# Kernel tuning notes

Hardware: AMD Instinct MI355X
Metric: run time of the kernel (lower is better)

The kernel has to match this reference:

```python
import jax, jax.numpy as jnp
import numpy as np

RATE = 2
KSIZE = 3
STRIDE = 1
SOFTMAX_SCALE = 10.0
EPS_NAN = 1e-4


def resize_bilinear_align(x, oh, ow):
    # torch F.interpolate(mode='bilinear', align_corners=True)
    B, C, H, W = x.shape
    ys = jnp.linspace(0.0, H - 1.0, oh)
    xs = jnp.linspace(0.0, W - 1.0, ow)
    y0 = jnp.floor(ys).astype(jnp.int32)
    y1 = jnp.minimum(y0 + 1, H - 1)
    wy = (ys - y0).astype(x.dtype)
    x0 = jnp.floor(xs).astype(jnp.int32)
    x1 = jnp.minimum(x0 + 1, W - 1)
    wx = (xs - x0).astype(x.dtype)
    t = x[:, :, y0, :] * (1 - wy)[None, None, :, None] + x[:, :, y1, :] * wy[None, None, :, None]
    return t[:, :, :, x0] * (1 - wx) + t[:, :, :, x1] * wx


def extract_patches(x, k, s, pad):
    # x: [C,H,W] -> [L, C, k, k] with SAME padding (pad on each side), L = oh*ow
    C, H, W = x.shape
    xp = jnp.pad(x, ((0, 0), (pad, pad), (pad, pad)))
    oh = (H + 2 * pad - k) // s + 1
    ow = (W + 2 * pad - k) // s + 1
    cols = jnp.stack(
        [xp[:, i:i + s * (oh - 1) + 1:s, j:j + s * (ow - 1) + 1:s]
         for i in range(k) for j in range(k)], axis=0)  # [k*k, C, oh, ow]
    return cols.reshape(k, k, C, oh, ow).transpose(3, 4, 2, 0, 1).reshape(oh * ow, C, k, k)


def conv2d(x, w, padding):
    # x: [N,C,H,W], w: [O,I,kh,kw]
    return jax.lax.conv_general_dilated(
        x, w, (1, 1), [(padding, padding)] * 2,
        dimension_numbers=('NCHW', 'OIHW', 'NCHW'))


def conv_transpose2d(x, w, stride, padding):
    # torch conv_transpose2d: x [N,I,h,w], w [I,O,kh,kw]
    k = w.shape[2]
    wt = jnp.flip(w, (2, 3)).transpose(1, 0, 2, 3)  # [O,I,kh,kw]
    return jax.lax.conv_general_dilated(
        x, wt, (1, 1), [(k - 1 - padding, k - 1 - padding)] * 2,
        lhs_dilation=(stride, stride),
        dimension_numbers=('NCHW', 'OIHW', 'NCHW'))


def setup_inputs() -> dict:
    key = jax.random.key(0)
    k1, k2 = jax.random.split(key)
    B, C, H, W = 4, 64, 128, 128
    background = jax.random.normal(k1, (B, C, H, W), dtype=jnp.float32)
    foreground = jax.random.normal(k2, (B, C, H, W), dtype=jnp.float32)
    return {"background": background, "foreground": foreground}


def reference(background, foreground):
    B, C, H, W = background.shape
    h, w = H // RATE, W // RATE
    fg = resize_bilinear_align(foreground, h, w)  # [B,C,h,w]
    bks = 2 * RATE  # background patch kernel = 4

    def per_sample(fg_i, bg_i):
        # foreground patches [L,C,3,3], L = h*w
        fgp = extract_patches(fg_i, KSIZE, STRIDE, 1)
        norm = jnp.sqrt(jnp.sum(fgp * fgp, axis=(1, 2, 3), keepdims=True))
        fgp_n = fgp / jnp.maximum(norm, EPS_NAN)
        # correlation score [1,L,h,w]
        score = conv2d(fg_i[None], fgp_n, padding=1)
        attn = jax.nn.softmax(score * SOFTMAX_SCALE, axis=1)
        attn = jnp.clip(attn, 1e-8, None)
        # background patches [L,C,4,4] (kernel 4, stride 2, same-pad 1)
        bgp = extract_patches(bg_i, bks, STRIDE * RATE, 1)
        out = conv_transpose2d(attn, bgp, stride=RATE, padding=1) / 4.0
        return out[0]  # [C,H,W]

    return jax.vmap(per_sample)(fg, background)
```

## Files before the change

kernel.cpp:

```cpp
#include <hip/hip_runtime.h>
#include <hip/hip_bf16.h>
#include <math.h>

#define B_  4
#define C_  64
#define H_  128
#define W_  128
#define HS  64
#define WS  64
#define L_  4096
#define K1  576
#define E2  1024
#define KSPLIT 1
#define ZLOG (-17.5f)

typedef _Float16 f16;
typedef f16 f16x8 __attribute__((ext_vector_type(8)));
typedef float f32x4 __attribute__((ext_vector_type(4)));

__device__ __forceinline__ void gload16(const void* g, void* l) {
    __builtin_amdgcn_global_load_lds(
        (const __attribute__((address_space(1))) unsigned int*)g,
        (__attribute__((address_space(3))) unsigned int*)l, 16, 0, 0);
}

__device__ __forceinline__ int swz(int r, int c) {
    return r * 128 + ((((c >> 3) ^ (r & 7)) << 3) | (c & 7));
}

__global__ __launch_bounds__(256) void resize_kernel(const float* __restrict__ fg,
                                                     float* __restrict__ fgs) {
    int idx = blockIdx.x * 256 + threadIdx.x;
    if (idx >= B_ * C_ * HS * WS) return;
    int j = idx & 63, i = (idx >> 6) & 63, bc = idx >> 12;
    const float sc = 127.0f / 63.0f;
    float yf = i * sc, xf = j * sc;
    int y0 = (int)floorf(yf); if (y0 > 127) y0 = 127;
    int x0 = (int)floorf(xf); if (x0 > 127) x0 = 127;
    int y1 = min(y0 + 1, 127), x1 = min(x0 + 1, 127);
    float wy = yf - (float)y0, wx = xf - (float)x0;
    const float* p = fg + (size_t)bc * (H_ * W_);
    float a = p[y0 * W_ + x0], b = p[y0 * W_ + x1];
    float c = p[y1 * W_ + x0], d = p[y1 * W_ + x1];
    float t0 = a * (1.f - wy) + c * wy;
    float t1 = b * (1.f - wy) + d * wy;
    fgs[idx] = t0 * (1.f - wx) + t1 * wx;
}

__global__ __launch_bounds__(256) void patch_kernel(const float* __restrict__ fgs,
                                                    f16* __restrict__ P_all) {
    int idx = blockIdx.x * 256 + threadIdx.x;
    int b = blockIdx.y;
    int k = idx % K1, l = idx / K1;
    int c = k / 9, r = k % 9;
    int dy = r / 3, dx = r % 3;
    int ly = l >> 6, lx = l & 63;
    int y = ly - 1 + dy, x = lx - 1 + dx;
    float v = 0.f;
    if ((unsigned)y < 64u && (unsigned)x < 64u)
        v = fgs[((size_t)b * C_ + c) * (HS * WS) + y * WS + x];
    P_all[(size_t)b * L_ * K1 + idx] = (f16)v;
}

__global__ __launch_bounds__(64) void norm_kernel(const f16* __restrict__ P_all,
                                                  float* __restrict__ nrm_all) {
    int l = blockIdx.x, b = blockIdx.y, t = threadIdx.x;
    const f16* row = P_all + ((size_t)b * L_ + l) * K1;
    float s = 0.f;
    for (int k = t; k < K1; k += 64) { float v = (float)row[k]; s = fmaf(v, v, s); }
    #pragma unroll
    for (int off = 32; off; off >>= 1) s += __shfl_down(s, off);
    if (t == 0) nrm_all[b * L_ + l] = fmaxf(sqrtf(s), 1e-4f);
}

__global__ __launch_bounds__(256) void v_kernel(const float* __restrict__ bg_g,
                                                f16* __restrict__ VT_g) {
    int ls = blockIdx.y;
    const float* bg_b = bg_g + (size_t)ls * (C_ * H_ * W_);
    f16* VT = VT_g + (size_t)ls * ((size_t)E2 * L_);
    int idx = blockIdx.x * 256 + threadIdx.x;
    int l = idx & 4095, e = idx >> 12;
    int c = e >> 4, r = e & 15;
    int ky = r >> 2, kx = r & 3;
    int ly = l >> 6, lx = l & 63;
    int by = 2 * ly - 1 + ky, bx = 2 * lx - 1 + kx;
    float v = 0.f;
    if ((unsigned)by < 128u && (unsigned)bx < 128u)
        v = bg_b[(size_t)c * (H_ * W_) + by * W_ + bx];
    VT[idx] = (f16)v;
}

__device__ __forceinline__ int nextk(int kn, int kLen, unsigned long long mask) {
    while (kn < kLen) {
        int t = kn >> 7;
        if (mask & (1ull << t)) return kn;
        unsigned long long m = mask >> t;
        if (!m) return kLen;
        kn = (t + __builtin_ctzll(m)) << 7;
    }
    return kn;
}

template <int EPI>
__global__ __launch_bounds__(256)
void mfma_gemm(const f16* __restrict__ A, size_t sA,
               const f16* __restrict__ Bt, size_t sB,
               int lda, int ldb, int kLen, void* __restrict__ outp, size_t sOut,
               int ldc, const float* __restrict__ nrm, float* __restrict__ rowsum,
               int* __restrict__ flags) {
    __shared__ __align__(16) f16 As[2][2][128 * 32];
    __shared__ __align__(16) f16 Bs[2][2][128 * 32];
    __shared__ float sred[8];

    const int lin = blockIdx.x;
    const int S = gridDim.x >> 3;
    int bx, by, ls;
    if (EPI == 1) {
        int s = (lin & 7) * S + (lin >> 3);
        int R = s / 136, q = s - R * 136;
        ls = R >> 2;
        int rr = R & 3;
        if (rr < 2) {
            int a = 0;
            while (q >= 16 - a) { q -= 16 - a; ++a; }
            by = a + (rr << 4); bx = a + q + (rr << 4);
        } else {
            if (q >= 128) return;
            by = q & 15; bx = 16 + ((rr & 1) << 3) + (q >> 4);
        }
    } else {
        int G = (lin & 7) * S + (lin >> 3);
        ls = G >> 8;
        by = (G >> 5) & 7; bx = G & 31;
    }

    A  += (size_t)ls * sA;
    Bt += (size_t)ls * sB;
    f16* outbase = (f16*)outp + (size_t)ls * sOut;
    if (EPI == 1) { nrm += (size_t)ls * L_; rowsum += (size_t)ls * L_; }
    flags += ls * 1024;

    const int tid = threadIdx.x;
    const int w = tid >> 6, lane = tid & 63;
    const int row0 = by * 128, col0 = bx * 128;

    unsigned long long kmask = ~0ull;
    if (EPI == 0) {
        int f = (lane < 32) ? flags[bx * 32 + lane] : 0;
        kmask = __ballot(f != 0);
    }

    const int srow = w * 32 + (lane >> 2);
    const int scol = (((lane & 3) ^ ((lane >> 3) & 3)) * 8);
    const f16* gA = A + (size_t)(row0 + srow) * lda + scol;
    const f16* gB = Bt + (size_t)(col0 + srow) * ldb + scol;
    const int l0 = (w * 32) * 32, l1 = (w * 32 + 16) * 32;

    const int wm = w >> 1, wn = w & 1;
    const int mfm = lane & 15, quad = lane >> 4;
    const int rq = (quad ^ ((mfm >> 1) & 3)) * 8;
    f32x4 acc[4][4] = {};

    int kc = (EPI == 0) ? nextk(0, kLen, kmask) : 0;
    if (kc < kLen) {
        int cur = 0;
        gload16(gA + kc,                         &As[0][0][l0]);
        gload16(gA + kc + (size_t)16 * lda,      &As[0][0][l1]);
        gload16(gA + kc + 32,                    &As[0][1][l0]);
        gload16(gA + kc + 32 + (size_t)16 * lda, &As[0][1][l1]);
        gload16(gB + kc,                         &Bs[0][0][l0]);
        gload16(gB + kc + (size_t)16 * ldb,      &Bs[0][0][l1]);
        gload16(gB + kc + 32,                    &Bs[0][1][l0]);
        gload16(gB + kc + 32 + (size_t)16 * ldb, &Bs[0][1][l1]);
        for (;;) {
            int kn = (EPI == 0) ? nextk(kc + 64, kLen, kmask) : kc + 64;
            __builtin_amdgcn_s_barrier();
            if (kn < kLen) {
                const int nxt = cur ^ 1;
                gload16(gA + kn,                         &As[nxt][0][l0]);
                gload16(gA + kn + (size_t)16 * lda,      &As[nxt][0][l1]);
                gload16(gA + kn + 32,                    &As[nxt][1][l0]);
                gload16(gA + kn + 32 + (size_t)16 * lda, &As[nxt][1][l1]);
                gload16(gB + kn,                         &Bs[nxt][0][l0]);
                gload16(gB + kn + (size_t)16 * ldb,      &Bs[nxt][0][l1]);
                gload16(gB + kn + 32,                    &Bs[nxt][1][l0]);
                gload16(gB + kn + 32 + (size_t)16 * ldb, &Bs[nxt][1][l1]);
                asm volatile("s_waitcnt vmcnt(8)" ::: "memory");
            } else {
                asm volatile("s_waitcnt vmcnt(0)" ::: "memory");
            }
            __builtin_amdgcn_s_barrier();
            __builtin_amdgcn_sched_barrier(0);
            #pragma unroll
            for (int h = 0; h < 2; ++h) {
                f16x8 af[4], bf[4];
                #pragma unroll
                for (int mi = 0; mi < 4; ++mi)
                    af[mi] = *(const f16x8*)&As[cur][h][(wm * 64 + mi * 16 + mfm) * 32 + rq];
                #pragma unroll
                for (int ni = 0; ni < 4; ++ni)
                    bf[ni] = *(const f16x8*)&Bs[cur][h][(wn * 64 + ni * 16 + mfm) * 32 + rq];
                __builtin_amdgcn_s_setprio(1);
                #pragma unroll
                for (int mi = 0; mi < 4; ++mi)
                    #pragma unroll
                    for (int ni = 0; ni < 4; ++ni)
                        acc[mi][ni] = __builtin_amdgcn_mfma_f32_16x16x32_f16(
                            af[mi], bf[ni], acc[mi][ni], 0, 0, 0);
                __builtin_amdgcn_s_setprio(0);
            }
            cur ^= 1;
            kc = kn;
            if (kc >= kLen) break;
        }
    }

    const int orow = row0 + wm * 64;
    const int ocol = col0 + wn * 64;
    f16* st = &As[0][0][0];

    if (EPI == 1) {
        f16* Eo = outbase;
        const bool offd = (by != bx);
        float rowm[16], cs[4], csr[16], cm2[4];
        #pragma unroll
        for (int j = 0; j < 16; ++j) {
            float n = nrm[orow + (j >> 2) * 16 + quad * 4 + (j & 3)];
            rowm[j] = 10.0f * n; csr[j] = 10.0f / n;
        }
        #pragma unroll
        for (int ni = 0; ni < 4; ++ni) {
            float n = nrm[ocol + ni * 16 + mfm];
            cs[ni] = 10.0f / n; cm2[ni] = 10.0f * n;
        }
        float mx1 = -1e30f, mx2 = -1e30f;
        #pragma unroll
        for (int ni = 0; ni < 4; ++ni)
            #pragma unroll
            for (int mi = 0; mi < 4; ++mi)
                #pragma unroll
                for (int r = 0; r < 4; ++r) {
                    float a = acc[mi][ni][r];
                    mx1 = fmaxf(mx1, a * cs[ni] - rowm[mi * 4 + r]);
                    mx2 = fmaxf(mx2, a * csr[mi * 4 + r] - cm2[ni]);
                }
        #pragma unroll
        for (int off = 32; off; off >>= 1) {
            mx1 = fmaxf(mx1, __shfl_xor(mx1, off));
            mx2 = fmaxf(mx2, __shfl_xor(mx2, off));
        }
        if (lane == 0) { sred[w] = mx1; sred[4 + w] = mx2; }
        __syncthreads();
        float b1 = fmaxf(fmaxf(sred[0], sred[1]), fmaxf(sred[2], sred[3]));
        float b2 = fmaxf(fmaxf(sred[4], sred[5]), fmaxf(sred[6], sred[7]));
        int nz1 = b1 > ZLOG;
        int nz2 = offd && (b2 > ZLOG);
        if (nz1) {
            float rs[16] = {};
            #pragma unroll
            for (int ni = 0; ni < 4; ++ni)
                #pragma unroll
                for (int mi = 0; mi < 4; ++mi)
                    #pragma unroll
                    for (int r = 0; r < 4; ++r) {
                        float e = __expf(acc[mi][ni][r] * cs[ni] - rowm[mi * 4 + r]);
                        rs[mi * 4 + r] += e;
                        st[swz(wm * 64 + mi * 16 + quad * 4 + r,
                               wn * 64 + ni * 16 + mfm)] = (f16)e;
                    }
            __syncthreads();
            #pragma unroll
            for (int it = 0; it < 8; ++it) {
                int chunk = it * 256 + tid;
                int row = chunk >> 4, c16 = chunk & 15;
                f16x8 v = *(const f16x8*)&st[row * 128 + ((c16 ^ (row & 7)) << 3)];
                *(f16x8*)&Eo[(size_t)(row0 + row) * ldc + col0 + c16 * 8] = v;
            }
            #pragma unroll
            for (int j = 0; j < 16; ++j) {
                float v = rs[j];
                v += __shfl_xor(v, 1); v += __shfl_xor(v, 2);
                v += __shfl_xor(v, 4); v += __shfl_xor(v, 8);
                if (mfm == 0)
                    atomicAdd(&rowsum[orow + (j >> 2) * 16 + quad * 4 + (j & 3)], v);
            }
        }
        if (nz2) {
            __syncthreads();
            float rs2[4] = {};
            #pragma unroll
            for (int ni = 0; ni < 4; ++ni)
                #pragma unroll
                for (int mi = 0; mi < 4; ++mi)
                    #pragma unroll
                    for (int r = 0; r < 4; ++r) {
                        float e = __expf(acc[mi][ni][r] * csr[mi * 4 + r] - cm2[ni]);
                        rs2[ni] += e;
                        st[swz(wn * 64 + ni * 16 + mfm,
                               wm * 64 + mi * 16 + quad * 4 + r)] = (f16)e;
                    }
            __syncthreads();
            #pragma unroll
            for (int it = 0; it < 8; ++it) {
                int chunk = it * 256 + tid;
                int row = chunk >> 4, c16 = chunk & 15;
                f16x8 v = *(const f16x8*)&st[row * 128 + ((c16 ^ (row & 7)) << 3)];
                *(f16x8*)&Eo[(size_t)(col0 + row) * ldc + row0 + c16 * 8] = v;
            }
            #pragma unroll
            for (int ni = 0; ni < 4; ++ni) {
                float v = rs2[ni];
                v += __shfl_xor(v, 16); v += __shfl_xor(v, 32);
                if (quad == 0)
                    atomicAdd(&rowsum[ocol + ni * 16 + mfm], v);
            }
        }
        if (tid == 0) {
            flags[by * 32 + bx] = nz1;
            if (offd) flags[bx * 32 + by] = nz2;
        }
    } else {
        __syncthreads();
        #pragma unroll
        for (int ni = 0; ni < 4; ++ni)
            #pragma unroll
            for (int mi = 0; mi < 4; ++mi)
                #pragma unroll
                for (int r = 0; r < 4; ++r)
                    st[swz(wm * 64 + mi * 16 + quad * 4 + r,
                           wn * 64 + ni * 16 + mfm)] = (f16)acc[mi][ni][r];
        __syncthreads();
        f16* base = outbase + (size_t)row0 * ldc + col0;
        #pragma unroll
        for (int it = 0; it < 8; ++it) {
            int chunk = it * 256 + tid;
            int row = chunk >> 4, c16 = chunk & 15;
            f16x8 v = *(const f16x8*)&st[row * 128 + ((c16 ^ (row & 7)) << 3)];
            *(f16x8*)&base[(size_t)row * ldc + c16 * 8] = v;
        }
    }
}

__global__ __launch_bounds__(256) void gather_kernel(const f16* __restrict__ OPT_g,
                                                     const float* __restrict__ rowsum_g,
                                                     float* __restrict__ out_g) {
    int ls = blockIdx.y;
    const f16* OPT = OPT_g + (size_t)ls * ((size_t)KSPLIT * E2 * L_);
    const float* rowsum = rowsum_g + (size_t)ls * L_;
    float* out_b = out_g + (size_t)ls * (C_ * H_ * W_);
    int idx = blockIdx.x * 256 + threadIdx.x;
    if (idx >= C_ * H_ * W_) return;
    int X = idx & 127, Y = (idx >> 7) & 127, c = idx >> 14;
    int kyp = (Y + 1) & 1;
    int kxp = (X + 1) & 1;
    float sum = 0.f;
    #pragma unroll
    for (int ky = kyp; ky < 4; ky += 2) {
        int py = (Y + 1 - ky) >> 1;
        if ((unsigned)py >= 64u) continue;
        #pragma unroll
        for (int kx = kxp; kx < 4; kx += 2) {
            int px = (X + 1 - kx) >> 1;
            if ((unsigned)px >= 64u) continue;
            int p = py * 64 + px;
            int e = c * 16 + ky * 4 + kx;
            float v = 0.f;
            #pragma unroll
            for (int s = 0; s < KSPLIT; ++s)
                v += (float)OPT[((size_t)s * E2 + e) * L_ + p];
            sum += v * __builtin_amdgcn_rcpf(rowsum[p]);
        }
    }
    out_b[idx] = 0.25f * sum;
}

extern "C" void kernel_launch(void* const* d_in, const int* in_sizes, int n_in,
                              void* d_out, int out_size, void* d_ws, size_t ws_size,
                              hipStream_t stream) {
    const float* bg = (const float*)d_in[0];
    const float* fg = (const float*)d_in[1];
    float* out = (float*)d_out;
    char* w8 = (char*)d_ws;

    float* fgs        = (float*)(w8);
    f16*   P_all      = (f16*)  (w8 + 4194304);
    float* nrm        = (float*)(w8 + 23068672);
    float* rowsum_all = (float*)(w8 + 23134208);
    int*   flags      = (int*)  (w8 + 23199744);
    const size_t base = 23216128;

    const size_t perVT  = (size_t)E2 * L_ * 2;
    const size_t perEb  = (size_t)L_ * L_ * 2;
    const size_t perOPT = (size_t)KSPLIT * E2 * L_ * 2;
    const size_t per = perVT + perEb + perOPT;
    int nb = 1;
    if (ws_size >= base + 4 * per) nb = 4;
    else if (ws_size >= base + 2 * per) nb = 2;

    f16* VT  = (f16*)(w8 + base);
    f16* Eb  = (f16*)(w8 + base + (size_t)nb * perVT);
    f16* OPT = (f16*)(w8 + base + (size_t)nb * (perVT + perEb));

    resize_kernel<<<(B_ * C_ * HS * WS) / 256, 256, 0, stream>>>(fg, fgs);
    patch_kernel<<<dim3((L_ * K1) / 256, B_), 256, 0, stream>>>(fgs, P_all);
    norm_kernel<<<dim3(L_, B_), 64, 0, stream>>>(P_all, nrm);
    hipMemsetAsync(rowsum_all, 0, (size_t)B_ * L_ * sizeof(float), stream);

    for (int g = 0; g < B_; g += nb) {
        const f16* P_g     = P_all + (size_t)g * L_ * K1;
        const float* nrm_g = nrm + (size_t)g * L_;
        float* rowsum_g    = rowsum_all + (size_t)g * L_;
        int* flags_g       = flags + g * 1024;

        v_kernel<<<dim3((L_ * E2) / 256, nb), 256, 0, stream>>>(
            bg + (size_t)g * C_ * H_ * W_, VT);

        mfma_gemm<1><<<544 * nb, 256, 0, stream>>>(
            P_g, (size_t)L_ * K1, P_g, (size_t)L_ * K1,
            K1, K1, K1, Eb, (size_t)L_ * L_, L_,
            nrm_g, rowsum_g, flags_g);

        mfma_gemm<0><<<256 * nb, 256, 0, stream>>>(
            VT, (size_t)E2 * L_, Eb, (size_t)L_ * L_,
            L_, L_, L_, OPT, (size_t)KSPLIT * E2 * L_, L_,
            nullptr, nullptr, flags_g);

        gather_kernel<<<dim3((C_ * H_ * W_) / 256, nb), 256, 0, stream>>>(
            OPT, rowsum_g, out + (size_t)g * C_ * H_ * W_);
    }
}
```

Before: 230.8 us.

## Use 512-thread blocks with 8 waves per 128x128 GEMM tile

Both MFMA GEMM kernels now run with 512 threads and 8 waves in a 2x4 wave grid. Each wave computes a 64x32 sub-tile instead of 64x64, so per-thread accumulators and global-to-LDS loads are halved. The softmax max reduction and the epilogue store loops are adjusted to match. The goal is more waves per CU to hide latency, at the cost of more LDS fragment reads per MFMA and heavier barrier synchronisation.

New measurement: 233.7 us. Within noise of the previous version (+1.3%).

```diff
diff --git a/kernel.cpp b/kernel.cpp
--- a/kernel.cpp
+++ b/kernel.cpp
@@ -102,7 +102,7 @@
 }
 
 template <int EPI>
-__global__ __launch_bounds__(256)
+__global__ __launch_bounds__(512, 4)
 void mfma_gemm(const f16* __restrict__ A, size_t sA,
                const f16* __restrict__ Bt, size_t sB,
                int lda, int ldb, int kLen, void* __restrict__ outp, size_t sOut,
@@ -110,7 +110,7 @@
                int* __restrict__ flags) {
     __shared__ __align__(16) f16 As[2][2][128 * 32];
     __shared__ __align__(16) f16 Bs[2][2][128 * 32];
-    __shared__ float sred[8];
+    __shared__ float sred[16];
 
     const int lin = blockIdx.x;
     const int S = gridDim.x >> 3;
@@ -150,42 +150,34 @@
         kmask = __ballot(f != 0);
     }
 
-    const int srow = w * 32 + (lane >> 2);
-    const int scol = (((lane & 3) ^ ((lane >> 3) & 3)) * 8);
+    const int srow = tid >> 2;
+    const int scol = (((tid & 3) ^ ((tid >> 3) & 3)) * 8);
     const f16* gA = A + (size_t)(row0 + srow) * lda + scol;
     const f16* gB = Bt + (size_t)(col0 + srow) * ldb + scol;
-    const int l0 = (w * 32) * 32, l1 = (w * 32 + 16) * 32;
-
-    const int wm = w >> 1, wn = w & 1;
+    const int ld = tid * 8;
+
+    const int wm = w >> 2, wn = w & 3;
     const int mfm = lane & 15, quad = lane >> 4;
     const int rq = (quad ^ ((mfm >> 1) & 3)) * 8;
-    f32x4 acc[4][4] = {};
+    f32x4 acc[4][2] = {};
 
     int kc = (EPI == 0) ? nextk(0, kLen, kmask) : 0;
     if (kc < kLen) {
         int cur = 0;
-        gload16(gA + kc,                         &As[0][0][l0]);
-        gload16(gA + kc + (size_t)16 * lda,      &As[0][0][l1]);
-        gload16(gA + kc + 32,                    &As[0][1][l0]);
-        gload16(gA + kc + 32 + (size_t)16 * lda, &As[0][1][l1]);
-        gload16(gB + kc,                         &Bs[0][0][l0]);
-        gload16(gB + kc + (size_t)16 * ldb,      &Bs[0][0][l1]);
-        gload16(gB + kc + 32,                    &Bs[0][1][l0]);
-        gload16(gB + kc + 32 + (size_t)16 * ldb, &Bs[0][1][l1]);
+        gload16(gA + kc,      &As[0][0][ld]);
+        gload16(gA + kc + 32, &As[0][1][ld]);
+        gload16(gB + kc,      &Bs[0][0][ld]);
+        gload16(gB + kc + 32, &Bs[0][1][ld]);
         for (;;) {
             int kn = (EPI == 0) ? nextk(kc + 64, kLen, kmask) : kc + 64;
             __builtin_amdgcn_s_barrier();
             if (kn < kLen) {
                 const int nxt = cur ^ 1;
-                gload16(gA + kn,                         &As[nxt][0][l0]);
-                gload16(gA + kn + (size_t)16 * lda,      &As[nxt][0][l1]);
-                gload16(gA + kn + 32,                    &As[nxt][1][l0]);
-                gload16(gA + kn + 32 + (size_t)16 * lda, &As[nxt][1][l1]);
-                gload16(gB + kn,                         &Bs[nxt][0][l0]);
-                gload16(gB + kn + (size_t)16 * ldb,      &Bs[nxt][0][l1]);
-                gload16(gB + kn + 32,                    &Bs[nxt][1][l0]);
-                gload16(gB + kn + 32 + (size_t)16 * ldb, &Bs[nxt][1][l1]);
-                asm volatile("s_waitcnt vmcnt(8)" ::: "memory");
+                gload16(gA + kn,      &As[nxt][0][ld]);
+                gload16(gA + kn + 32, &As[nxt][1][ld]);
+                gload16(gB + kn,      &Bs[nxt][0][ld]);
+                gload16(gB + kn + 32, &Bs[nxt][1][ld]);
+                asm volatile("s_waitcnt vmcnt(4)" ::: "memory");
             } else {
                 asm volatile("s_waitcnt vmcnt(0)" ::: "memory");
             }
@@ -193,18 +185,18 @@
             __builtin_amdgcn_sched_barrier(0);
             #pragma unroll
             for (int h = 0; h < 2; ++h) {
-                f16x8 af[4], bf[4];
+                f16x8 af[4], bf[2];
                 #pragma unroll
                 for (int mi = 0; mi < 4; ++mi)
                     af[mi] = *(const f16x8*)&As[cur][h][(wm * 64 + mi * 16 + mfm) * 32 + rq];
                 #pragma unroll
-                for (int ni = 0; ni < 4; ++ni)
-                    bf[ni] = *(const f16x8*)&Bs[cur][h][(wn * 64 + ni * 16 + mfm) * 32 + rq];
+                for (int ni = 0; ni < 2; ++ni)
+                    bf[ni] = *(const f16x8*)&Bs[cur][h][(wn * 32 + ni * 16 + mfm) * 32 + rq];
                 __builtin_amdgcn_s_setprio(1);
                 #pragma unroll
                 for (int mi = 0; mi < 4; ++mi)
                     #pragma unroll
-                    for (int ni = 0; ni < 4; ++ni)
+                    for (int ni = 0; ni < 2; ++ni)
                         acc[mi][ni] = __builtin_amdgcn_mfma_f32_16x16x32_f16(
                             af[mi], bf[ni], acc[mi][ni], 0, 0, 0);
                 __builtin_amdgcn_s_setprio(0);
@@ -216,26 +208,26 @@
     }
 
     const int orow = row0 + wm * 64;
-    const int ocol = col0 + wn * 64;
+    const int ocol = col0 + wn * 32;
     f16* st = &As[0][0][0];
 
     if (EPI == 1) {
         f16* Eo = outbase;
         const bool offd = (by != bx);
-        float rowm[16], cs[4], csr[16], cm2[4];
+        float rowm[16], csr[16], cs[2], cm2[2];
         #pragma unroll
         for (int j = 0; j < 16; ++j) {
             float n = nrm[orow + (j >> 2) * 16 + quad * 4 + (j & 3)];
             rowm[j] = 10.0f * n; csr[j] = 10.0f / n;
         }
         #pragma unroll
-        for (int ni = 0; ni < 4; ++ni) {
+        for (int ni = 0; ni < 2; ++ni) {
             float n = nrm[ocol + ni * 16 + mfm];
             cs[ni] = 10.0f / n; cm2[ni] = 10.0f * n;
         }
         float mx1 = -1e30f, mx2 = -1e30f;
         #pragma unroll
-        for (int ni = 0; ni < 4; ++ni)
+        for (int ni = 0; ni < 2; ++ni)
             #pragma unroll
             for (int mi = 0; mi < 4; ++mi)
                 #pragma unroll
@@ -249,16 +241,19 @@
             mx1 = fmaxf(mx1, __shfl_xor(mx1, off));
             mx2 = fmaxf(mx2, __shfl_xor(mx2, off));
         }
-        if (lane == 0) { sred[w] = mx1; sred[4 + w] = mx2; }
+        if (lane == 0) { sred[w] = mx1; sred[8 + w] = mx2; }
         __syncthreads();
-        float b1 = fmaxf(fmaxf(sred[0], sred[1]), fmaxf(sred[2], sred[3]));
-        float b2 = fmaxf(fmaxf(sred[4], sred[5]), fmaxf(sred[6], sred[7]));
+        float b1 = sred[0], b2 = sred[8];
+        #pragma unroll
+        for (int k = 1; k < 8; ++k) {
+            b1 = fmaxf(b1, sred[k]); b2 = fmaxf(b2, sred[8 + k]);
+        }
         int nz1 = b1 > ZLOG;
         int nz2 = offd && (b2 > ZLOG);
         if (nz1) {
             float rs[16] = {};
             #pragma unroll
-            for (int ni = 0; ni < 4; ++ni)
+            for (int ni = 0; ni < 2; ++ni)
                 #pragma unroll
                 for (int mi = 0; mi < 4; ++mi)
                     #pragma unroll
@@ -266,12 +261,12 @@
                         float e = __expf(acc[mi][ni][r] * cs[ni] - rowm[mi * 4 + r]);
                         rs[mi * 4 + r] += e;
                         st[swz(wm * 64 + mi * 16 + quad * 4 + r,
-                               wn * 64 + ni * 16 + mfm)] = (f16)e;
+                               wn * 32 + ni * 16 + mfm)] = (f16)e;
                     }
             __syncthreads();
             #pragma unroll
-            for (int it = 0; it < 8; ++it) {
-                int chunk = it * 256 + tid;
+            for (int it = 0; it < 4; ++it) {
+                int chunk = it * 512 + tid;
                 int row = chunk >> 4, c16 = chunk & 15;
                 f16x8 v = *(const f16x8*)&st[row * 128 + ((c16 ^ (row & 7)) << 3)];
                 *(f16x8*)&Eo[(size_t)(row0 + row) * ldc + col0 + c16 * 8] = v;
@@ -287,28 +282,28 @@
         }
         if (nz2) {
             __syncthreads();
-            float rs2[4] = {};
-            #pragma unroll
-            for (int ni = 0; ni < 4; ++ni)
+            float rs2[2] = {};
+            #pragma unroll
+            for (int ni = 0; ni < 2; ++ni)
                 #pragma unroll
                 for (int mi = 0; mi < 4; ++mi)
                     #pragma unroll
                     for (int r = 0; r < 4; ++r) {
                         float e = __expf(acc[mi][ni][r] * csr[mi * 4 + r] - cm2[ni]);
                         rs2[ni] += e;
-                        st[swz(wn * 64 + ni * 16 + mfm,
+                        st[swz(wn * 32 + ni * 16 + mfm,
                                wm * 64 + mi * 16 + quad * 4 + r)] = (f16)e;
                     }
             __syncthreads();
             #pragma unroll
-            for (int it = 0; it < 8; ++it) {
-                int chunk = it * 256 + tid;
+            for (int it = 0; it < 4; ++it) {
+                int chunk = it * 512 + tid;
                 int row = chunk >> 4, c16 = chunk & 15;
                 f16x8 v = *(const f16x8*)&st[row * 128 + ((c16 ^ (row & 7)) << 3)];
                 *(f16x8*)&Eo[(size_t)(col0 + row) * ldc + row0 + c16 * 8] = v;
             }
             #pragma unroll
-            for (int ni = 0; ni < 4; ++ni) {
+            for (int ni = 0; ni < 2; ++ni) {
                 float v = rs2[ni];
                 v += __shfl_xor(v, 16); v += __shfl_xor(v, 32);
                 if (quad == 0)
@@ -322,18 +317,18 @@
     } else {
         __syncthreads();
         #pragma unroll
-        for (int ni = 0; ni < 4; ++ni)
+        for (int ni = 0; ni < 2; ++ni)
             #pragma unroll
             for (int mi = 0; mi < 4; ++mi)
                 #pragma unroll
                 for (int r = 0; r < 4; ++r)
                     st[swz(wm * 64 + mi * 16 + quad * 4 + r,
-                           wn * 64 + ni * 16 + mfm)] = (f16)acc[mi][ni][r];
+                           wn * 32 + ni * 16 + mfm)] = (f16)acc[mi][ni][r];
         __syncthreads();
         f16* base = outbase + (size_t)row0 * ldc + col0;
         #pragma unroll
-        for (int it = 0; it < 8; ++it) {
-            int chunk = it * 256 + tid;
+        for (int it = 0; it < 4; ++it) {
+            int chunk = it * 512 + tid;
             int row = chunk >> 4, c16 = chunk & 15;
             f16x8 v = *(const f16x8*)&st[row * 128 + ((c16 ^ (row & 7)) << 3)];
             *(f16x8*)&base[(size_t)row * ldc + c16 * 8] = v;
@@ -415,12 +410,12 @@
         v_kernel<<<dim3((L_ * E2) / 256, nb), 256, 0, stream>>>(
             bg + (size_t)g * C_ * H_ * W_, VT);
 
-        mfma_gemm<1><<<544 * nb, 256, 0, stream>>>(
+        mfma_gemm<1><<<544 * nb, 512, 0, stream>>>(
             P_g, (size_t)L_ * K1, P_g, (size_t)L_ * K1,
             K1, K1, K1, Eb, (size_t)L_ * L_, L_,
             nrm_g, rowsum_g, flags_g);
 
-        mfma_gemm<0><<<256 * nb, 256, 0, stream>>>(
+        mfma_gemm<0><<<256 * nb, 512, 0, stream>>>(
             VT, (size_t)E2 * L_, Eb, (size_t)L_ * L_,
             L_, L_, L_, OPT, (size_t)KSPLIT * E2 * L_, L_,
             nullptr, nullptr, flags_g);
```
